# Kernel optimization log

Measured on AMD Instinct MI355X. Metric: run time of the kernel, lower is better.

## Reference

```python
import jax, jax.numpy as jnp
import numpy as np

EPS = 1e-5
K = 64  # nsample

def lrelu(x):
    return jnp.where(x > 0, x, 0.1 * x)

def bn_eval(x, g, b):
    # eval-mode BatchNorm1d with running_mean=0, running_var=1
    return x * (g / jnp.sqrt(1.0 + EPS))[None, :, None] + b[None, :, None]


def setup_inputs() -> dict:
    key = jax.random.key(0)
    ks = jax.random.split(key, 32)
    B, N1, N2, C, LC = 128, 21, 4096, 256, 256
    H = LC // 2  # 128
    s = 0.05
    inp = {
        'xyz1': jax.random.normal(ks[0], (B, 3, N1), jnp.float32),
        'xyz2': jax.random.normal(ks[1], (B, 3, N2), jnp.float32),
        'points1': jax.random.normal(ks[2], (B, LC, N1), jnp.float32),
        'points2': jax.random.normal(ks[3], (B, C, N2), jnp.float32),
        'bf_w1': jax.random.normal(ks[4], (H, LC), jnp.float32) * s,
        'bf_bias1': jax.random.normal(ks[5], (H, N1), jnp.float32) * s,
        'bf_g1': jnp.ones((H,), jnp.float32),
        'bf_be1': jnp.zeros((H,), jnp.float32),
        'bf_w2': jax.random.normal(ks[6], (H, H), jnp.float32) * s,
        'bf_bias2': jax.random.normal(ks[7], (H, N1), jnp.float32) * s,
        'bf_g2': jnp.ones((H,), jnp.float32),
        'bf_be2': jnp.zeros((H,), jnp.float32),
        'bf_w3': jax.random.normal(ks[8], (H, H), jnp.float32) * s,
        'bf_bias3': jax.random.normal(ks[9], (H, N1), jnp.float32) * s,
        'bf_g3': jnp.ones((H,), jnp.float32),
        'bf_be3': jnp.zeros((H,), jnp.float32),
        # mlp (Conv2d 1x1 with bias): in = 256 + 128 + 3 = 387
        'mlp_w1': jax.random.normal(ks[10], (256, C + H + 3), jnp.float32) * s,
        'mlp_b1': jnp.zeros((256,), jnp.float32),
        'mlp_w2': jax.random.normal(ks[11], (256, 256), jnp.float32) * s,
        'mlp_b2': jnp.zeros((256,), jnp.float32),
        'mlp_w3': jax.random.normal(ks[12], (256, 256), jnp.float32) * s,
        'mlp_b3': jnp.zeros((256,), jnp.float32),
        # mlp2 (Conv1d 1x1, no bias)
        'mlp2_w1': jax.random.normal(ks[13], (256, 256), jnp.float32) * s,
        'mlp2_w2': jax.random.normal(ks[14], (256, 256), jnp.float32) * s,
        'reg_w': jax.random.normal(ks[15], (3, 256), jnp.float32) * s,
        'reg_b': jnp.zeros((3,), jnp.float32),
    }
    return inp


def reference(xyz1, xyz2, points1, points2,
              bf_w1, bf_bias1, bf_g1, bf_be1,
              bf_w2, bf_bias2, bf_g2, bf_be2,
              bf_w3, bf_bias3, bf_g3, bf_be3,
              mlp_w1, mlp_b1, mlp_w2, mlp_b2, mlp_w3, mlp_b3,
              mlp2_w1, mlp2_w2, reg_w, reg_b):
    # --- biasfold on joint features [B, LC, N1] ---
    x = points1
    for w, bb, g, be in ((bf_w1, bf_bias1, bf_g1, bf_be1),
                         (bf_w2, bf_bias2, bf_g2, bf_be2),
                         (bf_w3, bf_bias3, bf_g3, bf_be3)):
        x = lrelu(bn_eval(jnp.einsum('oc,bcn->bon', w, x) + bb[None], g, be))
    p1 = x.transpose(0, 2, 1)            # [B, N1, 128]

    x1 = xyz1.transpose(0, 2, 1)         # [B, N1, 3]
    x2 = xyz2.transpose(0, 2, 1)         # [B, N2, 3]
    p2 = points2.transpose(0, 2, 1)      # [B, N2, C]

    # --- squared pairwise distance + kNN ---
    sqr = (jnp.sum(x1 ** 2, -1)[:, :, None]
           + jnp.sum(x2 ** 2, -1)[:, None, :]
           - 2.0 * jnp.einsum('bnc,bmc->bnm', x1, x2))   # [B, N1, N2]
    _, knn_idx = jax.lax.top_k(-sqr, K)                  # [B, N1, K]

    gather = jax.vmap(lambda pts, idx: pts[idx])
    neighbor_xyz = gather(x2, knn_idx)                   # [B, N1, K, 3]
    direction_xyz = neighbor_xyz - x1[:, :, None, :]
    g2 = gather(p2, knn_idx)                             # [B, N1, K, C]
    g1 = jnp.broadcast_to(p1[:, :, None, :], knn_idx.shape + (p1.shape[-1],))
    feat = jnp.concatenate([g1, g2, direction_xyz], -1)  # [B, N1, K, 387]

    # --- shared 1x1 conv MLP (channels-last einsum) ---
    for w, b in ((mlp_w1, mlp_b1), (mlp_w2, mlp_b2), (mlp_w3, mlp_b3)):
        feat = lrelu(jnp.einsum('oc,bnkc->bnko', w, feat) + b)

    pooled = jnp.max(feat, axis=2)                       # [B, N1, 256] max over K

    for w in (mlp2_w1, mlp2_w2):
        pooled = lrelu(jnp.einsum('oc,bnc->bno', w, pooled))

    out = jnp.einsum('oc,bnc->bno', reg_w, pooled) + reg_b  # [B, N1, 3]
    return out.transpose(0, 2, 1)                           # [B, 3, N1]
```

## Files before the change

### kernel.cpp

```cpp
#include <hip/hip_runtime.h>
#include <float.h>

#define BB 128
#define N1 21
#define N2 4096
#define CC 256
#define LCH 256
#define HH 128
#define KNN 64
#define KP 268

typedef _Float16 f16;
typedef f16 f16x4 __attribute__((ext_vector_type(4)));
typedef f16 f16x8 __attribute__((ext_vector_type(8)));
typedef float f32x4 __attribute__((ext_vector_type(4)));

static const size_t OFF_A1   = 0;
static const size_t OFF_KNN  = OFF_A1 + (size_t)BB * N1 * 256;
static const size_t OFF_W4T  = OFF_KNN + (size_t)BB * N1 * KNN;
static const size_t OFF_W5T  = OFF_W4T + 65536;
static const size_t OFF_P1H  = OFF_W5T + 65536;
static const size_t OFF_P2H  = OFF_P1H + 32768;
static const size_t OFF_P3H  = OFF_P2H + 32768;
static const size_t OFF_USED = OFF_P3H + 32768;
static const size_t OFF_P2T  = OFF_USED + 131072;

__device__ __forceinline__ float lrelu(float x) { return x > 0.f ? x : 0.1f * x; }
__device__ __forceinline__ unsigned short bits16(f16 h) { unsigned short r; __builtin_memcpy(&r, &h, 2); return r; }


__device__ __forceinline__ void pack_one(int e, const float* __restrict__ w, int stride, int koff,
                                         f16* __restrict__ hi) {
  int j = e & 7, lane = (e >> 3) & 63, ntg = (e >> 9) & 15, ks = e >> 13;
  int n = ntg * 16 + (lane & 15);
  int k = ks * 32 + 4 * (lane >> 4) + (j & 3) + 16 * (j >> 2);
  hi[e] = (f16)w[(size_t)n * stride + koff + k];
}

__global__ __launch_bounds__(256) void k_pack(
    const float* __restrict__ w1, const float* __restrict__ w2,
    const float* __restrict__ w3, const float* __restrict__ w4,
    const float* __restrict__ w5, float* __restrict__ ws) {
  int t = blockIdx.x * 256 + threadIdx.x;
  if (t < 131072) {
    int m = t >> 16, v = t & 65535;
    int c = v >> 8, o = v & 255;
    const float* src = m ? w5 : w4;
    float* dst = ws + (m ? OFF_W5T : OFF_W4T);
    dst[v] = src[o * 256 + c];
    return;
  }
  int u = t - 131072;
  if (u < 65536) { pack_one(u, w1, 387, 128, (f16*)(ws + OFF_P1H)); return; }
  u -= 65536;
  if (u < 65536) { pack_one(u, w2, 256, 0, (f16*)(ws + OFF_P2H)); return; }
  u -= 65536;
  if (u < 65536) { pack_one(u, w3, 256, 0, (f16*)(ws + OFF_P3H)); return; }
}

__global__ __launch_bounds__(256) void k_zero(unsigned int* __restrict__ used32) {
  used32[blockIdx.x * 256 + threadIdx.x] = 0;
}

__global__ __launch_bounds__(128) void k_biasfold(
    const float* __restrict__ points1,
    const float* __restrict__ w1, const float* __restrict__ bb1,
    const float* __restrict__ g1, const float* __restrict__ be1,
    const float* __restrict__ w2, const float* __restrict__ bb2,
    const float* __restrict__ g2, const float* __restrict__ be2,
    const float* __restrict__ w3, const float* __restrict__ bb3,
    const float* __restrict__ g3, const float* __restrict__ be3,
    const float* __restrict__ w1mlp,
    float* __restrict__ A1out) {
  int blk = blockIdx.x;
  int b = blk / N1, n = blk % N1;
  int t = threadIdx.x;
  __shared__ float x0[LCH], x1s[HH], x2s[HH], x3s[HH];
  const float bnS = 1.0f / sqrtf(1.0f + 1e-5f);

  x0[t]       = points1[((size_t)b * LCH + t) * N1 + n];
  x0[t + 128] = points1[((size_t)b * LCH + t + 128) * N1 + n];
  __syncthreads();
  {
    float acc = 0.f;
    const float* wr = w1 + (size_t)t * LCH;
    #pragma unroll 4
    for (int c = 0; c < LCH; c++) acc += wr[c] * x0[c];
    acc += bb1[t * N1 + n];
    acc = acc * (g1[t] * bnS) + be1[t];
    x1s[t] = lrelu(acc);
  }
  __syncthreads();
  {
    float acc = 0.f;
    const float* wr = w2 + (size_t)t * HH;
    #pragma unroll 4
    for (int c = 0; c < HH; c++) acc += wr[c] * x1s[c];
    acc += bb2[t * N1 + n];
    acc = acc * (g2[t] * bnS) + be2[t];
    x2s[t] = lrelu(acc);
  }
  __syncthreads();
  {
    float acc = 0.f;
    const float* wr = w3 + (size_t)t * HH;
    #pragma unroll 4
    for (int c = 0; c < HH; c++) acc += wr[c] * x2s[c];
    acc += bb3[t * N1 + n];
    acc = acc * (g3[t] * bnS) + be3[t];
    x3s[t] = lrelu(acc);
  }
  __syncthreads();
  #pragma unroll
  for (int rep = 0; rep < 2; rep++) {
    int o = t + rep * 128;
    const float* wr = w1mlp + (size_t)o * 387;
    float acc = 0.f;
    #pragma unroll 4
    for (int c = 0; c < HH; c++) acc += wr[c] * x3s[c];
    A1out[(size_t)blk * 256 + o] = acc;
  }
}

__global__ __launch_bounds__(256) void k_knn(
    const float* __restrict__ xyz1, const float* __restrict__ xyz2,
    int* __restrict__ knn, unsigned char* __restrict__ used) {
  int blk = blockIdx.x;
  int b = blk / N1, n = blk % N1;
  int t = threadIdx.x;
  __shared__ float wvv[2][4];
  __shared__ int wii[2][4];

  float ax = xyz1[((size_t)b * 3 + 0) * N1 + n];
  float ay = xyz1[((size_t)b * 3 + 1) * N1 + n];
  float az = xyz1[((size_t)b * 3 + 2) * N1 + n];
  float xx1 = ax * ax + ay * ay + az * az;
  const float* X = xyz2 + (size_t)b * 3 * N2;

  float dl[16];
  #pragma unroll
  for (int i = 0; i < 16; i++) {
    int j = t + i * 256;
    float px = X[j], py = X[N2 + j], pz = X[2 * N2 + j];
    float xx2 = px * px + py * py + pz * pz;
    float dot = ax * px + ay * py + az * pz;
    dl[i] = (xx1 + xx2) - 2.0f * dot;
  }

  int* out = knn + (size_t)blk * KNN;
  unsigned char* ub = used + (size_t)b * N2;
  for (int it = 0; it < KNN; it++) {
    float best = dl[0]; int bs = 0;
    #pragma unroll
    for (int i = 1; i < 16; i++)
      if (dl[i] < best) { best = dl[i]; bs = i; }
    int bi = t + bs * 256;
    #pragma unroll
    for (int off = 32; off; off >>= 1) {
      float ov = __shfl_down(best, off);
      int oi = __shfl_down(bi, off);
      if (ov < best || (ov == best && oi < bi)) { best = ov; bi = oi; }
    }
    int w = t >> 6;
    int sl = it & 1;
    if ((t & 63) == 0) { wvv[sl][w] = best; wii[sl][w] = bi; }
    __syncthreads();
    float bv = wvv[sl][0]; int bj = wii[sl][0];
    #pragma unroll
    for (int p = 1; p < 4; p++)
      if (wvv[sl][p] < bv || (wvv[sl][p] == bv && wii[sl][p] < bj)) { bv = wvv[sl][p]; bj = wii[sl][p]; }
    if (t == 0) { out[it] = bj; ub[bj] = 1; }
    if ((bj & 255) == t) {
      int slot = bj >> 8;
      #pragma unroll
      for (int i = 0; i < 16; i++)
        if (i == slot) dl[i] = FLT_MAX;
    }
  }
}

__global__ __launch_bounds__(256) void k_t2(
    const float* __restrict__ points2, unsigned short* __restrict__ p2t,
    const unsigned char* __restrict__ used) {
  __shared__ unsigned short tile[64][66];
  int bid = blockIdx.x;
  int b = bid >> 8;
  int rem = bid & 255;
  int n0 = (rem >> 2) << 6;
  int c0 = (rem & 3) << 6;
  int t = threadIdx.x;
  int tl = t & 63, tg = t >> 6;

  const float* src = points2 + ((size_t)b * CC) * N2;
  float v[16];
  #pragma unroll
  for (int i = 0; i < 16; i++)
    v[i] = src[(size_t)(c0 + tg * 16 + i) * N2 + n0 + tl];
  #pragma unroll
  for (int i = 0; i < 16; i++)
    tile[tg * 16 + i][tl] = bits16((f16)v[i]);

  uint4 ubv = *(const uint4*)(used + (size_t)b * N2 + n0 + tg * 16);
  const unsigned char* ubb = (const unsigned char*)&ubv;

  __syncthreads();
  unsigned short* dst = p2t + ((size_t)b * N2) * CC;
  unsigned short o[16];
  #pragma unroll
  for (int i = 0; i < 16; i++) o[i] = tile[tl][tg * 16 + i];
  #pragma unroll
  for (int i = 0; i < 16; i++)
    if (ubb[i])
      dst[(size_t)(n0 + tg * 16 + i) * CC + c0 + tl] = o[i];
}

__device__ __forceinline__ void run_layer64(
    const f16* __restrict__ BH, const f16* Xh,
    int w, int lane, int r16, int g, f32x4 acc[4][4]) {
  #pragma unroll 1
  for (int ks = 0; ks < 8; ks++) {
    f16x8 Bh[4];
    #pragma unroll
    for (int nt = 0; nt < 4; nt++) {
      size_t fi = ((size_t)((ks * 16 + w * 4 + nt) * 64 + lane)) * 8;
      Bh[nt] = *(const f16x8*)(BH + fi);
    }
    int k0 = ks * 32 + 4 * g;
    f16x8 Ah[4];
    #pragma unroll
    for (int mt = 0; mt < 4; mt++) {
      int base = (mt * 16 + r16) * KP + k0;
      f16x4 h0 = *(const f16x4*)(Xh + base);
      f16x4 h1 = *(const f16x4*)(Xh + base + 16);
      Ah[mt] = __builtin_shufflevector(h0, h1, 0, 1, 2, 3, 4, 5, 6, 7);
    }
    #pragma unroll
    for (int mt = 0; mt < 4; mt++)
      #pragma unroll
      for (int nt = 0; nt < 4; nt++)
        acc[mt][nt] = __builtin_amdgcn_mfma_f32_16x16x32_f16(Ah[mt], Bh[nt], acc[mt][nt], 0, 0, 0);
  }
}

__device__ __forceinline__ void writeback_act64(
    f32x4 acc[4][4], const float* __restrict__ bias,
    f16* Xh, int w, int r16, int g) {
  #pragma unroll
  for (int nt = 0; nt < 4; nt++) {
    int nl = w * 64 + nt * 16 + r16;
    float bv = bias[nl];
    #pragma unroll
    for (int mt = 0; mt < 4; mt++)
      #pragma unroll
      for (int j = 0; j < 4; j++) {
        int m = mt * 16 + 4 * g + j;
        Xh[m * KP + nl] = (f16)lrelu(acc[mt][nt][j] + bv);
      }
  }
}

template <int TRANS>
__global__ __launch_bounds__(256) void k_fused9(
    const float* __restrict__ xyz1, const float* __restrict__ xyz2,
    const float* __restrict__ points2, const unsigned short* __restrict__ p2t,
    const float* __restrict__ A1ws, const int* __restrict__ knn,
    const float* __restrict__ w1mlp,
    const f16* __restrict__ P1H, const f16* __restrict__ P2H,
    const f16* __restrict__ P3H,
    const float* __restrict__ b1, const float* __restrict__ b2,
    const float* __restrict__ b3,
    const float* __restrict__ W4T, const float* __restrict__ W5T,
    const float* __restrict__ regw, const float* __restrict__ regb,
    float* __restrict__ out) {
  int bid = blockIdx.x;
  int xcd = bid & 7, slot = bid >> 3;
  int b = xcd * 16 + slot / 21;
  int n1 = slot % 21;
  int row = b * N1 + n1;

  int t = threadIdx.x;
  int lane = t & 63, w = t >> 6;
  int r16 = lane & 15, g = lane >> 4;

  __shared__ __align__(16) f16 Xhi[64 * KP];
  __shared__ float dirs[64][3];
  __shared__ int idxs[KNN];
  __shared__ float x1p[3];

  if (t < KNN) idxs[t] = knn[(size_t)row * KNN + t];
  if (t < 3) x1p[t] = xyz1[((size_t)b * 3 + t) * N1 + n1];
  __syncthreads();

  if (TRANS) {
    int r = t >> 2, qq = t & 3;
    int id = idxs[r];
    const uint4* src = (const uint4*)(p2t + ((size_t)b * N2 + id) * CC + qq * 64);
    #pragma unroll
    for (int i = 0; i < 8; i++) {
      uint4 v = src[i];
      f16x8 val;
      __builtin_memcpy(&val, &v, 16);
      f16x4 lo4 = __builtin_shufflevector(val, val, 0, 1, 2, 3);
      f16x4 hi4 = __builtin_shufflevector(val, val, 4, 5, 6, 7);
      int cpos = r * KP + qq * 64 + i * 8;
      *(f16x4*)(Xhi + cpos) = lo4;
      *(f16x4*)(Xhi + cpos + 4) = hi4;
    }
  } else {
    int r = t >> 2, qq = t & 3;
    int id = idxs[r];
    const float* src = points2 + (size_t)b * CC * N2 + id;
    #pragma unroll 4
    for (int i = 0; i < 64; i++) {
      int c = qq * 64 + i;
      Xhi[r * KP + c] = (f16)src[(size_t)c * N2];
    }
  }
  const float* x2b = xyz2 + (size_t)b * 3 * N2;
  if (t < 64) {
    int id = idxs[t];
    #pragma unroll
    for (int d = 0; d < 3; d++)
      dirs[t][d] = x2b[(size_t)d * N2 + id] - x1p[d];
  }

  float a1v[4], wd0[4], wd1[4], wd2[4];
  #pragma unroll
  for (int nt = 0; nt < 4; nt++) {
    int n = w * 64 + nt * 16 + r16;
    a1v[nt] = A1ws[(size_t)row * 256 + n];
    wd0[nt] = w1mlp[(size_t)n * 387 + 384];
    wd1[nt] = w1mlp[(size_t)n * 387 + 385];
    wd2[nt] = w1mlp[(size_t)n * 387 + 386];
  }
  __syncthreads();

  f32x4 acc[4][4];
  #pragma unroll
  for (int mt = 0; mt < 4; mt++)
    #pragma unroll
    for (int nt = 0; nt < 4; nt++)
      #pragma unroll
      for (int j = 0; j < 4; j++) {
        int m = mt * 16 + 4 * g + j;
        acc[mt][nt][j] = a1v[nt] + wd0[nt] * dirs[m][0]
                                 + wd1[nt] * dirs[m][1]
                                 + wd2[nt] * dirs[m][2];
      }
  run_layer64(P1H, Xhi, w, lane, r16, g, acc);
  __syncthreads();
  writeback_act64(acc, b1, Xhi, w, r16, g);
  __syncthreads();

  #pragma unroll
  for (int mt = 0; mt < 4; mt++)
    #pragma unroll
    for (int nt = 0; nt < 4; nt++) acc[mt][nt] = (f32x4){0.f, 0.f, 0.f, 0.f};
  run_layer64(P2H, Xhi, w, lane, r16, g, acc);
  __syncthreads();
  writeback_act64(acc, b2, Xhi, w, r16, g);
  __syncthreads();

  #pragma unroll
  for (int mt = 0; mt < 4; mt++)
    #pragma unroll
    for (int nt = 0; nt < 4; nt++) acc[mt][nt] = (f32x4){0.f, 0.f, 0.f, 0.f};
  run_layer64(P3H, Xhi, w, lane, r16, g, acc);

  float poolm[4];
  #pragma unroll
  for (int nt = 0; nt < 4; nt++) {
    float m = -FLT_MAX;
    #pragma unroll
    for (int mt = 0; mt < 4; mt++)
      #pragma unroll
      for (int j = 0; j < 4; j++) m = fmaxf(m, acc[mt][nt][j]);
    m = fmaxf(m, __shfl_xor(m, 16));
    m = fmaxf(m, __shfl_xor(m, 32));
    poolm[nt] = m;
  }
  __syncthreads();

  float* fb = (float*)Xhi;
  if (g == 0) {
    #pragma unroll
    for (int nt = 0; nt < 4; nt++) {
      int n = w * 64 + nt * 16 + r16;
      fb[n] = lrelu(poolm[nt] + b3[n]);
    }
  }
  __syncthreads();
  {
    float a = 0.f;
    #pragma unroll 4
    for (int c = 0; c < 256; c++) a += W4T[(size_t)c * 256 + t] * fb[c];
    fb[256 + t] = lrelu(a);
  }
  __syncthreads();
  {
    float a = 0.f;
    #pragma unroll 4
    for (int c = 0; c < 256; c++) a += W5T[(size_t)c * 256 + t] * fb[256 + c];
    fb[512 + t] = lrelu(a);
  }
  __syncthreads();
  if (t < 192) {
    int o = t >> 6;
    float a = 0.f;
    #pragma unroll
    for (int i = 0; i < 4; i++) {
      int c = (t & 63) + 64 * i;
      a += regw[o * 256 + c] * fb[512 + c];
    }
    #pragma unroll
    for (int off = 32; off; off >>= 1) a += __shfl_xor(a, off);
    if ((t & 63) == 0) out[((size_t)b * 3 + o) * N1 + n1] = a + regb[o];
  }
}

extern "C" void kernel_launch(void* const* d_in, const int* in_sizes, int n_in,
                              void* d_out, int out_size, void* d_ws, size_t ws_size,
                              hipStream_t stream) {
  const float* xyz1    = (const float*)d_in[0];
  const float* xyz2    = (const float*)d_in[1];
  const float* points1 = (const float*)d_in[2];
  const float* points2 = (const float*)d_in[3];
  const float* bf_w1 = (const float*)d_in[4],  *bf_b1 = (const float*)d_in[5];
  const float* bf_g1 = (const float*)d_in[6],  *bf_e1 = (const float*)d_in[7];
  const float* bf_w2 = (const float*)d_in[8],  *bf_b2 = (const float*)d_in[9];
  const float* bf_g2 = (const float*)d_in[10], *bf_e2 = (const float*)d_in[11];
  const float* bf_w3 = (const float*)d_in[12], *bf_b3 = (const float*)d_in[13];
  const float* bf_g3 = (const float*)d_in[14], *bf_e3 = (const float*)d_in[15];
  const float* mlp_w1 = (const float*)d_in[16], *mlp_b1 = (const float*)d_in[17];
  const float* mlp_w2 = (const float*)d_in[18], *mlp_b2 = (const float*)d_in[19];
  const float* mlp_w3 = (const float*)d_in[20], *mlp_b3 = (const float*)d_in[21];
  const float* mlp2_w1 = (const float*)d_in[22], *mlp2_w2 = (const float*)d_in[23];
  const float* reg_w = (const float*)d_in[24], *reg_b = (const float*)d_in[25];

  float* ws  = (float*)d_ws;
  float* A1  = ws + OFF_A1;
  int*   knn = (int*)(ws + OFF_KNN);
  unsigned char* used = (unsigned char*)(ws + OFF_USED);
  unsigned short* p2t = (unsigned short*)(ws + OFF_P2T);

  float* out = (float*)d_out;
  int rows = BB * N1;

  size_t need_bytes = OFF_P2T * sizeof(float) + (size_t)BB * N2 * CC * sizeof(unsigned short);
  bool use_trans = (ws_size >= need_bytes);

  k_pack<<<1280, 256, 0, stream>>>(mlp_w1, mlp_w2, mlp_w3, mlp2_w1, mlp2_w2, ws);
  k_biasfold<<<rows, 128, 0, stream>>>(points1,
      bf_w1, bf_b1, bf_g1, bf_e1,
      bf_w2, bf_b2, bf_g2, bf_e2,
      bf_w3, bf_b3, bf_g3, bf_e3, mlp_w1, A1);
  k_zero<<<512, 256, 0, stream>>>((unsigned int*)used);
  k_knn<<<rows, 256, 0, stream>>>(xyz1, xyz2, knn, used);
  if (use_trans) {
    k_t2<<<BB * 256, 256, 0, stream>>>(points2, p2t, used);
    k_fused9<1><<<rows, 256, 0, stream>>>(xyz1, xyz2, points2, p2t, A1, knn, mlp_w1,
        (const f16*)(ws + OFF_P1H), (const f16*)(ws + OFF_P2H), (const f16*)(ws + OFF_P3H),
        mlp_b1, mlp_b2, mlp_b3,
        ws + OFF_W4T, ws + OFF_W5T, reg_w, reg_b, out);
  } else {
    k_fused9<0><<<rows, 256, 0, stream>>>(xyz1, xyz2, points2, p2t, A1, knn, mlp_w1,
        (const f16*)(ws + OFF_P1H), (const f16*)(ws + OFF_P2H), (const f16*)(ws + OFF_P3H),
        mlp_b1, mlp_b2, mlp_b3,
        ws + OFF_W4T, ws + OFF_W5T, reg_w, reg_b, out);
  }
}
```

Measured before the change: 657.4 us.

## Merge prep kernels into one launch and double-buffer MFMA fragment loads

Folds the weight-packing, used-mask zeroing and biasfold kernels into a single launch that dispatches on block index, removing two kernel launches and their gaps. The MFMA layer loop now prefetches the next k-step's A and B fragments into a second register set while the current step's MFMAs issue, hiding load latency. The extra fragment registers raise VGPR pressure and could lower occupancy. The biasfold blocks now run 256 threads with half of them idle for most phases.

```diff
diff --git a/kernel.cpp b/kernel.cpp
--- a/kernel.cpp
+++ b/kernel.cpp
@@ -37,32 +37,11 @@
   hi[e] = (f16)w[(size_t)n * stride + koff + k];
 }
 
-__global__ __launch_bounds__(256) void k_pack(
-    const float* __restrict__ w1, const float* __restrict__ w2,
-    const float* __restrict__ w3, const float* __restrict__ w4,
-    const float* __restrict__ w5, float* __restrict__ ws) {
-  int t = blockIdx.x * 256 + threadIdx.x;
-  if (t < 131072) {
-    int m = t >> 16, v = t & 65535;
-    int c = v >> 8, o = v & 255;
-    const float* src = m ? w5 : w4;
-    float* dst = ws + (m ? OFF_W5T : OFF_W4T);
-    dst[v] = src[o * 256 + c];
-    return;
-  }
-  int u = t - 131072;
-  if (u < 65536) { pack_one(u, w1, 387, 128, (f16*)(ws + OFF_P1H)); return; }
-  u -= 65536;
-  if (u < 65536) { pack_one(u, w2, 256, 0, (f16*)(ws + OFF_P2H)); return; }
-  u -= 65536;
-  if (u < 65536) { pack_one(u, w3, 256, 0, (f16*)(ws + OFF_P3H)); return; }
-}
-
-__global__ __launch_bounds__(256) void k_zero(unsigned int* __restrict__ used32) {
-  used32[blockIdx.x * 256 + threadIdx.x] = 0;
-}
-
-__global__ __launch_bounds__(128) void k_biasfold(
+__global__ __launch_bounds__(256) void k_prep0(
+    const float* __restrict__ mw1, const float* __restrict__ mw2,
+    const float* __restrict__ mw3, const float* __restrict__ mw4,
+    const float* __restrict__ mw5, float* __restrict__ ws,
+    unsigned int* __restrict__ used32,
     const float* __restrict__ points1,
     const float* __restrict__ w1, const float* __restrict__ bb1,
     const float* __restrict__ g1, const float* __restrict__ be1,
@@ -70,55 +49,81 @@
     const float* __restrict__ g2, const float* __restrict__ be2,
     const float* __restrict__ w3, const float* __restrict__ bb3,
     const float* __restrict__ g3, const float* __restrict__ be3,
-    const float* __restrict__ w1mlp,
     float* __restrict__ A1out) {
-  int blk = blockIdx.x;
-  int b = blk / N1, n = blk % N1;
+  __shared__ float x0[LCH], x1s[HH], x2s[HH], x3s[HH];
+  int bid = blockIdx.x;
   int t = threadIdx.x;
-  __shared__ float x0[LCH], x1s[HH], x2s[HH], x3s[HH];
-  const float bnS = 1.0f / sqrtf(1.0f + 1e-5f);
-
-  x0[t]       = points1[((size_t)b * LCH + t) * N1 + n];
-  x0[t + 128] = points1[((size_t)b * LCH + t + 128) * N1 + n];
-  __syncthreads();
+
+  if (bid < 1280) {
+    int e = bid * 256 + t;
+    if (e < 131072) {
+      int m = e >> 16, v = e & 65535;
+      int c = v >> 8, o = v & 255;
+      const float* src = m ? mw5 : mw4;
+      float* dst = ws + (m ? OFF_W5T : OFF_W4T);
+      dst[v] = src[o * 256 + c];
+      return;
+    }
+    int u = e - 131072;
+    if (u < 65536) { pack_one(u, mw1, 387, 128, (f16*)(ws + OFF_P1H)); return; }
+    u -= 65536;
+    if (u < 65536) { pack_one(u, mw2, 256, 0, (f16*)(ws + OFF_P2H)); return; }
+    u -= 65536;
+    if (u < 65536) { pack_one(u, mw3, 256, 0, (f16*)(ws + OFF_P3H)); return; }
+    return;
+  }
+  bid -= 1280;
+  if (bid < 512) {
+    used32[bid * 256 + t] = 0;
+    return;
+  }
+  bid -= 512;
   {
-    float acc = 0.f;
-    const float* wr = w1 + (size_t)t * LCH;
-    #pragma unroll 4
-    for (int c = 0; c < LCH; c++) acc += wr[c] * x0[c];
-    acc += bb1[t * N1 + n];
-    acc = acc * (g1[t] * bnS) + be1[t];
-    x1s[t] = lrelu(acc);
-  }
-  __syncthreads();
-  {
-    float acc = 0.f;
-    const float* wr = w2 + (size_t)t * HH;
-    #pragma unroll 4
-    for (int c = 0; c < HH; c++) acc += wr[c] * x1s[c];
-    acc += bb2[t * N1 + n];
-    acc = acc * (g2[t] * bnS) + be2[t];
-    x2s[t] = lrelu(acc);
-  }
-  __syncthreads();
-  {
-    float acc = 0.f;
-    const float* wr = w3 + (size_t)t * HH;
-    #pragma unroll 4
-    for (int c = 0; c < HH; c++) acc += wr[c] * x2s[c];
-    acc += bb3[t * N1 + n];
-    acc = acc * (g3[t] * bnS) + be3[t];
-    x3s[t] = lrelu(acc);
-  }
-  __syncthreads();
-  #pragma unroll
-  for (int rep = 0; rep < 2; rep++) {
-    int o = t + rep * 128;
-    const float* wr = w1mlp + (size_t)o * 387;
-    float acc = 0.f;
-    #pragma unroll 4
-    for (int c = 0; c < HH; c++) acc += wr[c] * x3s[c];
-    A1out[(size_t)blk * 256 + o] = acc;
+    int blk = bid;
+    int b = blk / N1, n = blk % N1;
+    const float bnS = 1.0f / sqrtf(1.0f + 1e-5f);
+    if (t < 128) {
+      x0[t]       = points1[((size_t)b * LCH + t) * N1 + n];
+      x0[t + 128] = points1[((size_t)b * LCH + t + 128) * N1 + n];
+    }
+    __syncthreads();
+    if (t < 128) {
+      float acc = 0.f;
+      const float* wr = w1 + (size_t)t * LCH;
+      #pragma unroll 4
+      for (int c = 0; c < LCH; c++) acc += wr[c] * x0[c];
+      acc += bb1[t * N1 + n];
+      acc = acc * (g1[t] * bnS) + be1[t];
+      x1s[t] = lrelu(acc);
+    }
+    __syncthreads();
+    if (t < 128) {
+      float acc = 0.f;
+      const float* wr = w2 + (size_t)t * HH;
+      #pragma unroll 4
+      for (int c = 0; c < HH; c++) acc += wr[c] * x1s[c];
+      acc += bb2[t * N1 + n];
+      acc = acc * (g2[t] * bnS) + be2[t];
+      x2s[t] = lrelu(acc);
+    }
+    __syncthreads();
+    if (t < 128) {
+      float acc = 0.f;
+      const float* wr = w3 + (size_t)t * HH;
+      #pragma unroll 4
+      for (int c = 0; c < HH; c++) acc += wr[c] * x2s[c];
+      acc += bb3[t * N1 + n];
+      acc = acc * (g3[t] * bnS) + be3[t];
+      x3s[t] = lrelu(acc);
+    }
+    __syncthreads();
+    {
+      const float* wr = mw1 + (size_t)t * 387;
+      float acc = 0.f;
+      #pragma unroll 4
+      for (int c = 0; c < HH; c++) acc += wr[c] * x3s[c];
+      A1out[(size_t)blk * 256 + t] = acc;
+    }
   }
 }
 
@@ -214,31 +219,48 @@
       dst[(size_t)(n0 + tg * 16 + i) * CC + c0 + tl] = o[i];
 }
 
+__device__ __forceinline__ void load_Bfrag(const f16* __restrict__ BH, int ks, int w, int lane,
+                                           f16x8 B[4]) {
+  #pragma unroll
+  for (int nt = 0; nt < 4; nt++) {
+    size_t fi = ((size_t)((ks * 16 + w * 4 + nt) * 64 + lane)) * 8;
+    B[nt] = *(const f16x8*)(BH + fi);
+  }
+}
+__device__ __forceinline__ void load_Afrag(const f16* Xh, int ks, int r16, int g, f16x8 A[4]) {
+  int k0 = ks * 32 + 4 * g;
+  #pragma unroll
+  for (int mt = 0; mt < 4; mt++) {
+    int base = (mt * 16 + r16) * KP + k0;
+    f16x4 h0 = *(const f16x4*)(Xh + base);
+    f16x4 h1 = *(const f16x4*)(Xh + base + 16);
+    A[mt] = __builtin_shufflevector(h0, h1, 0, 1, 2, 3, 4, 5, 6, 7);
+  }
+}
+__device__ __forceinline__ void mfma16(f16x8 A[4], f16x8 B[4], f32x4 acc[4][4]) {
+  #pragma unroll
+  for (int mt = 0; mt < 4; mt++)
+    #pragma unroll
+    for (int nt = 0; nt < 4; nt++)
+      acc[mt][nt] = __builtin_amdgcn_mfma_f32_16x16x32_f16(A[mt], B[nt], acc[mt][nt], 0, 0, 0);
+}
+
 __device__ __forceinline__ void run_layer64(
     const f16* __restrict__ BH, const f16* Xh,
     int w, int lane, int r16, int g, f32x4 acc[4][4]) {
+  f16x8 B0[4], A0[4], B1[4], A1f[4];
+  load_Bfrag(BH, 0, w, lane, B0);
+  load_Afrag(Xh, 0, r16, g, A0);
   #pragma unroll 1
-  for (int ks = 0; ks < 8; ks++) {
-    f16x8 Bh[4];
-    #pragma unroll
-    for (int nt = 0; nt < 4; nt++) {
-      size_t fi = ((size_t)((ks * 16 + w * 4 + nt) * 64 + lane)) * 8;
-      Bh[nt] = *(const f16x8*)(BH + fi);
-    }
-    int k0 = ks * 32 + 4 * g;
-    f16x8 Ah[4];
-    #pragma unroll
-    for (int mt = 0; mt < 4; mt++) {
-      int base = (mt * 16 + r16) * KP + k0;
-      f16x4 h0 = *(const f16x4*)(Xh + base);
-      f16x4 h1 = *(const f16x4*)(Xh + base + 16);
-      Ah[mt] = __builtin_shufflevector(h0, h1, 0, 1, 2, 3, 4, 5, 6, 7);
-    }
-    #pragma unroll
-    for (int mt = 0; mt < 4; mt++)
-      #pragma unroll
-      for (int nt = 0; nt < 4; nt++)
-        acc[mt][nt] = __builtin_amdgcn_mfma_f32_16x16x32_f16(Ah[mt], Bh[nt], acc[mt][nt], 0, 0, 0);
+  for (int ks = 0; ks < 8; ks += 2) {
+    load_Bfrag(BH, ks + 1, w, lane, B1);
+    load_Afrag(Xh, ks + 1, r16, g, A1f);
+    mfma16(A0, B0, acc);
+    if (ks + 2 < 8) {
+      load_Bfrag(BH, ks + 2, w, lane, B0);
+      load_Afrag(Xh, ks + 2, r16, g, A0);
+    }
+    mfma16(A1f, B1, acc);
   }
 }
 
@@ -260,7 +282,7 @@
 }
 
 template <int TRANS>
-__global__ __launch_bounds__(256) void k_fused9(
+__global__ __launch_bounds__(256) void k_fused10(
     const float* __restrict__ xyz1, const float* __restrict__ xyz2,
     const float* __restrict__ points2, const unsigned short* __restrict__ p2t,
     const float* __restrict__ A1ws, const int* __restrict__ knn,
@@ -449,21 +471,21 @@
   size_t need_bytes = OFF_P2T * sizeof(float) + (size_t)BB * N2 * CC * sizeof(unsigned short);
   bool use_trans = (ws_size >= need_bytes);
 
-  k_pack<<<1280, 256, 0, stream>>>(mlp_w1, mlp_w2, mlp_w3, mlp2_w1, mlp2_w2, ws);
-  k_biasfold<<<rows, 128, 0, stream>>>(points1,
+  k_prep0<<<4480, 256, 0, stream>>>(
+      mlp_w1, mlp_w2, mlp_w3, mlp2_w1, mlp2_w2, ws, (unsigned int*)used,
+      points1,
       bf_w1, bf_b1, bf_g1, bf_e1,
       bf_w2, bf_b2, bf_g2, bf_e2,
-      bf_w3, bf_b3, bf_g3, bf_e3, mlp_w1, A1);
-  k_zero<<<512, 256, 0, stream>>>((unsigned int*)used);
+      bf_w3, bf_b3, bf_g3, bf_e3, A1);
   k_knn<<<rows, 256, 0, stream>>>(xyz1, xyz2, knn, used);
   if (use_trans) {
     k_t2<<<BB * 256, 256, 0, stream>>>(points2, p2t, used);
-    k_fused9<1><<<rows, 256, 0, stream>>>(xyz1, xyz2, points2, p2t, A1, knn, mlp_w1,
+    k_fused10<1><<<rows, 256, 0, stream>>>(xyz1, xyz2, points2, p2t, A1, knn, mlp_w1,
         (const f16*)(ws + OFF_P1H), (const f16*)(ws + OFF_P2H), (const f16*)(ws + OFF_P3H),
         mlp_b1, mlp_b2, mlp_b3,
         ws + OFF_W4T, ws + OFF_W5T, reg_w, reg_b, out);
   } else {
-    k_fused9<0><<<rows, 256, 0, stream>>>(xyz1, xyz2, points2, p2t, A1, knn, mlp_w1,
+    k_fused10<0><<<rows, 256, 0, stream>>>(xyz1, xyz2, points2, p2t, A1, knn, mlp_w1,
         (const f16*)(ws + OFF_P1H), (const f16*)(ws + OFF_P2H), (const f16*)(ws + OFF_P3H),
         mlp_b1, mlp_b2, mlp_b3,
         ws + OFF_W4T, ws + OFF_W5T, reg_w, reg_b, out);
```

Result: slower. 696.6 us (+6.0%).
